# Kernel optimization log

Hardware: AMD Instinct MI355X
Metric: run time of the kernel (lower is better)

Reference implementation:

```python
import jax, jax.numpy as jnp
import numpy as np

NUM_HEADS = 4


def setup_inputs() -> dict:
    key = jax.random.key(0)
    ks = jax.random.split(key, 12)
    N, E_edges, ND, ED, D, G = 50000, 800000, 128, 64, 256, 128
    h = jax.random.normal(ks[0], (N, ND), dtype=jnp.float32)
    edge_index = jax.random.randint(ks[1], (2, E_edges), 0, N)
    edge_attr = jax.random.normal(ks[2], (E_edges, ED), dtype=jnp.float32)
    batch = jnp.sort(jax.random.randint(ks[3], (N,), 0, G))
    node_w = jax.random.normal(ks[4], (D, ND), dtype=jnp.float32) / np.sqrt(ND)
    node_b = jnp.zeros((D,), dtype=jnp.float32)
    edge_w = jax.random.normal(ks[5], (D, ED), dtype=jnp.float32) / np.sqrt(ED)
    edge_b = jnp.zeros((D,), dtype=jnp.float32)
    query = jax.random.normal(ks[6], (1, D), dtype=jnp.float32)
    in_w = jax.random.normal(ks[7], (3 * D, D), dtype=jnp.float32) / np.sqrt(D)
    in_b = jnp.zeros((3 * D,), dtype=jnp.float32)
    out_w = jax.random.normal(ks[8], (D, D), dtype=jnp.float32) / np.sqrt(D)
    out_b = jnp.zeros((D,), dtype=jnp.float32)
    return {"h": h, "edge_index": edge_index, "edge_attr": edge_attr, "batch": batch,
            "num_graphs": G, "node_w": node_w, "node_b": node_b,
            "edge_w": edge_w, "edge_b": edge_b, "query": query,
            "in_w": in_w, "in_b": in_b, "out_w": out_w, "out_b": out_b}


def reference(h, edge_index, edge_attr, batch, num_graphs,
              node_w, node_b, edge_w, edge_b, query, in_w, in_b, out_w, out_b):
    N = h.shape[0]
    D = query.shape[-1]
    dh = D // NUM_HEADS
    G = num_graphs
    # node projection
    h_proj = h @ node_w.T + node_b  # [N, D]
    # scatter-mean edge features to source nodes
    row = edge_index[0]
    e_proj = edge_attr @ edge_w.T + edge_b  # [E, D]
    e_sum = jax.ops.segment_sum(e_proj, row, num_segments=N)
    cnt = jax.ops.segment_sum(jnp.ones((row.shape[0],), jnp.float32), row, num_segments=N)
    h_proj = h_proj + e_sum / jnp.maximum(cnt, 1.0)[:, None]
    # per-graph single-query multi-head attention (torch MultiheadAttention math)
    wq, wk, wv = in_w[:D], in_w[D:2 * D], in_w[2 * D:]
    bq, bk, bv = in_b[:D], in_b[D:2 * D], in_b[2 * D:]
    q = (query @ wq.T + bq).reshape(NUM_HEADS, dh)            # [H, dh]
    k = (h_proj @ wk.T + bk).reshape(N, NUM_HEADS, dh)        # [N, H, dh]
    v = (h_proj @ wv.T + bv).reshape(N, NUM_HEADS, dh)        # [N, H, dh]
    scores = jnp.einsum('hd,nhd->nh', q, k) / jnp.sqrt(jnp.float32(dh))  # [N, H]
    smax = jax.ops.segment_max(scores, batch, num_segments=G)  # [G, H]
    w = jnp.exp(scores - smax[batch])                          # [N, H]
    denom = jax.ops.segment_sum(w, batch, num_segments=G)      # [G, H]
    p = w / jnp.maximum(denom[batch], 1e-30)                   # [N, H]
    pooled = jax.ops.segment_sum(p[:, :, None] * v, batch, num_segments=G)  # [G, H, dh]
    out = pooled.reshape(G, 1, D) @ out_w.T + out_b            # [G, 1, D]
    return out
```

## Files before the change

kernel.cpp:

```cpp
#include <hip/hip_runtime.h>
#include <hip/hip_bf16.h>
#include <math.h>

#define NDIM 128
#define EDIM 64
#define DDIM 256
#define BM 32
#define APK_STRIDE 204
#define HPB_STRIDE 264
#define NSPLIT 4
#define CAP 96
#define NSWZ (8 * 12 * 64 * 8)

typedef __attribute__((ext_vector_type(8))) short short8;
typedef __attribute__((ext_vector_type(16))) float floatx16;

__device__ inline ushort f2bf(float x) {
    uint32_t u = __float_as_uint(x);
    uint32_t r = (u + 0x7fff + ((u >> 16) & 1)) >> 16;
    return (ushort)r;
}
__device__ inline float bf2f(ushort h) { return __uint_as_float(((uint32_t)h) << 16); }
__device__ inline uint32_t pack_hilo(float x) {
    ushort hi = f2bf(x);
    ushort lo = f2bf(x - bf2f(hi));
    return (uint32_t)hi | ((uint32_t)lo << 16);
}

__global__ __launch_bounds__(256) void k_setup(
    int* __restrict__ zero_p, int n_zero, int ZBLK,
    const float* __restrict__ node_w, const float* __restrict__ edge_w,
    ushort* __restrict__ whi, ushort* __restrict__ wlo,
    const float* __restrict__ query, const float* __restrict__ in_w,
    const float* __restrict__ in_b, float* __restrict__ qk, float* __restrict__ sb)
{
    const int tid = threadIdx.x;
    int b = blockIdx.x;
    if (b < ZBLK) {
        int i = b * 256 + tid;
        if (i < n_zero) zero_p[i] = 0;
        return;
    }
    b -= ZBLK;
    if (b < 192) {
        int idx = b * 256 + tid;
        int i = idx & 7;
        int l = (idx >> 3) & 63;
        int rest = idx >> 9;
        int s = rest % 12;
        int t2 = rest / 12;
        int k = s * 16 + (l >> 5) * 8 + i;
        int col = t2 * 32 + (l & 31);
        float val = (k < NDIM) ? node_w[(size_t)col * NDIM + k]
                               : edge_w[(size_t)col * EDIM + (k - NDIM)];
        ushort hi = f2bf(val);
        ushort lo = f2bf(val - bf2f(hi));
        whi[idx] = hi;
        wlo[idx] = lo;
        return;
    }
    __shared__ float q_s[DDIM];
    __shared__ float qv[DDIM];
    q_s[tid] = query[tid];
    __syncthreads();
    float acc = in_b[tid];
    const float* wq = in_w + (size_t)tid * DDIM;
    for (int i = 0; i < DDIM; ++i) acc += q_s[i] * wq[i];
    qv[tid] = acc;
    __syncthreads();
    for (int h = 0; h < 4; ++h) {
        float a = 0.f;
        for (int d = 0; d < 64; ++d)
            a += qv[h * 64 + d] * in_w[(size_t)(DDIM + h * 64 + d) * DDIM + tid];
        qk[h * DDIM + tid] = a;
    }
    if (tid < 4) {
        float a = 0.f;
        for (int d = 0; d < 64; ++d) a += qv[tid * 64 + d] * in_b[DDIM + tid * 64 + d];
        sb[tid] = a;
    }
}

__global__ __launch_bounds__(256) void k_scatbin(
    const int* __restrict__ erow, const float* __restrict__ edge_attr,
    int* __restrict__ fill, ushort* __restrict__ ebin, int E)
{
    int gid = blockIdx.x * 256 + threadIdx.x;
    int e = gid >> 3;
    int seg8 = gid & 7;
    if (e >= E) return;
    int r = erow[e];
    int pos = 0;
    if (seg8 == 0) pos = atomicAdd(&fill[r], 1);
    pos = __shfl(pos, 0, 8);
    if (pos >= CAP) return;
    const float* ea = edge_attr + (size_t)e * EDIM + seg8 * 8;
    float4 va = *reinterpret_cast<const float4*>(ea);
    float4 vb = *reinterpret_cast<const float4*>(ea + 4);
    short8 o;
    o[0] = (short)f2bf(va.x); o[1] = (short)f2bf(va.y);
    o[2] = (short)f2bf(va.z); o[3] = (short)f2bf(va.w);
    o[4] = (short)f2bf(vb.x); o[5] = (short)f2bf(vb.y);
    o[6] = (short)f2bf(vb.z); o[7] = (short)f2bf(vb.w);
    *reinterpret_cast<short8*>(
        ebin + ((size_t)r * CAP + pos) * EDIM + seg8 * 8) = o;
}

__global__ __launch_bounds__(256) void k_projagg(
    const float* __restrict__ h, const ushort* __restrict__ ebin,
    const int* __restrict__ fill,
    const ushort* __restrict__ whi, const ushort* __restrict__ wlo,
    const float* __restrict__ node_b, const float* __restrict__ edge_b,
    const float* __restrict__ qk, const float* __restrict__ sb,
    ushort* __restrict__ h_proj_bf, float* __restrict__ scores, int N)
{
    extern __shared__ char smem[];
    uint32_t* A_pk = (uint32_t*)smem;
    ushort*   hpbuf = (ushort*)smem;
    __shared__ float qk_s[4 * DDIM];
    __shared__ float cnt_s[BM];
    __shared__ float sb_s[4];

    const int tid = threadIdx.x;
    const int n0 = blockIdx.x * BM;

    if (tid < BM) {
        int n = n0 + tid;
        cnt_s[tid] = (n < N) ? (float)fill[n] : 0.f;
    }
    if (tid < 4) sb_s[tid] = sb[tid];
    for (int i = tid; i < 4 * DDIM; i += 256) qk_s[i] = qk[i];

    const float4* h4 = reinterpret_cast<const float4*>(h);
#pragma unroll
    for (int it = 0; it < 4; ++it) {
        int idx4 = tid + 256 * it;
        int node = idx4 >> 5;
        int kq = idx4 & 31;
        float4 v = make_float4(0.f, 0.f, 0.f, 0.f);
        if (n0 + node < N) v = h4[(size_t)(n0 + node) * 32 + kq];
        uint32_t* dst = &A_pk[node * APK_STRIDE + kq * 4];
        dst[0] = pack_hilo(v.x); dst[1] = pack_hilo(v.y);
        dst[2] = pack_hilo(v.z); dst[3] = pack_hilo(v.w);
    }

    __syncthreads();

    {
        int node = tid >> 3;
        int seg8 = tid & 7;
        int n = n0 + node;
        float a[8];
#pragma unroll
        for (int i = 0; i < 8; ++i) a[i] = 0.f;
        if (n < N) {
            int c = min((int)cnt_s[node], CAP);
            const ushort* eb = ebin + ((size_t)n * CAP) * EDIM + seg8 * 8;
            int j = 0;
            for (; j + 3 < c; j += 4) {
                short8 v0 = *reinterpret_cast<const short8*>(eb + (size_t)(j + 0) * EDIM);
                short8 v1 = *reinterpret_cast<const short8*>(eb + (size_t)(j + 1) * EDIM);
                short8 v2 = *reinterpret_cast<const short8*>(eb + (size_t)(j + 2) * EDIM);
                short8 v3 = *reinterpret_cast<const short8*>(eb + (size_t)(j + 3) * EDIM);
#pragma unroll
                for (int i = 0; i < 8; ++i)
                    a[i] += (bf2f((ushort)v0[i]) + bf2f((ushort)v1[i]))
                          + (bf2f((ushort)v2[i]) + bf2f((ushort)v3[i]));
            }
            for (; j < c; ++j) {
                short8 v0 = *reinterpret_cast<const short8*>(eb + (size_t)j * EDIM);
#pragma unroll
                for (int i = 0; i < 8; ++i) a[i] += bf2f((ushort)v0[i]);
            }
        }
        float inv = 1.f / fmaxf(cnt_s[node], 1.f);
        uint32_t* dst = &A_pk[node * APK_STRIDE + NDIM + seg8 * 8];
#pragma unroll
        for (int i = 0; i < 8; ++i) dst[i] = pack_hilo(a[i] * inv);
    }
    __syncthreads();

    const int lane = tid & 63;
    const int w = tid >> 6;
    const int kg8 = (lane >> 5) * 8;
    const uint32_t* arow_p = &A_pk[(lane & 31) * APK_STRIDE];

    floatx16 acc[2];
#pragma unroll
    for (int t = 0; t < 2; ++t) acc[t] = 0.f;

#pragma unroll 4
    for (int s = 0; s < 12; ++s) {
        uint32_t au[8];
        *reinterpret_cast<uint4*>(&au[0]) = *reinterpret_cast<const uint4*>(&arow_p[s * 16 + kg8]);
        *reinterpret_cast<uint4*>(&au[4]) = *reinterpret_cast<const uint4*>(&arow_p[s * 16 + kg8 + 4]);
        short8 ahi, alo;
#pragma unroll
        for (int j = 0; j < 8; ++j) {
            ahi[j] = (short)(au[j] & 0xffffu);
            alo[j] = (short)(au[j] >> 16);
        }
#pragma unroll
        for (int t = 0; t < 2; ++t) {
            size_t boff = ((size_t)(((w * 2 + t) * 12 + s) * 64) + lane) * 8;
            short8 bhi = *reinterpret_cast<const short8*>(whi + boff);
            short8 blo = *reinterpret_cast<const short8*>(wlo + boff);
            acc[t] = __builtin_amdgcn_mfma_f32_32x32x16_bf16(ahi, bhi, acc[t], 0, 0, 0);
            acc[t] = __builtin_amdgcn_mfma_f32_32x32x16_bf16(ahi, blo, acc[t], 0, 0, 0);
            acc[t] = __builtin_amdgcn_mfma_f32_32x32x16_bf16(alo, bhi, acc[t], 0, 0, 0);
        }
    }
    __syncthreads();

#pragma unroll
    for (int t = 0; t < 2; ++t) {
        int colt = (w * 2 + t) * 32 + (lane & 31);
        float nb = node_b[colt];
        float eb = edge_b[colt];
#pragma unroll
        for (int r = 0; r < 16; ++r) {
            int row = (r & 3) + 8 * (r >> 2) + 4 * (lane >> 5);
            float fl = (cnt_s[row] >= 0.5f) ? 1.f : 0.f;
            float hp = acc[t][r] + nb + fl * eb;
            hpbuf[row * HPB_STRIDE + colt] = f2bf(hp);
        }
    }
    __syncthreads();

    {
        int row = tid >> 3, seg = tid & 7;
        int n = n0 + row;
        float s0 = 0.f, s1 = 0.f, s2 = 0.f, s3 = 0.f;
#pragma unroll
        for (int q = 0; q < 4; ++q) {
            short8 v = *reinterpret_cast<const short8*>(
                &hpbuf[row * HPB_STRIDE + seg * 32 + q * 8]);
#pragma unroll
            for (int jj = 0; jj < 8; ++jj) {
                float hv = bf2f((ushort)v[jj]);
                int dim = seg * 32 + q * 8 + jj;
                s0 += hv * qk_s[0 * DDIM + dim];
                s1 += hv * qk_s[1 * DDIM + dim];
                s2 += hv * qk_s[2 * DDIM + dim];
                s3 += hv * qk_s[3 * DDIM + dim];
            }
            if (n < N)
                *reinterpret_cast<short8*>(
                    &h_proj_bf[(size_t)n * DDIM + seg * 32 + q * 8]) = v;
        }
#pragma unroll
        for (int off = 1; off < 8; off <<= 1) {
            s0 += __shfl_xor(s0, off);
            s1 += __shfl_xor(s1, off);
            s2 += __shfl_xor(s2, off);
            s3 += __shfl_xor(s3, off);
        }
        if (seg == 0 && n < N) {
            scores[(size_t)n * 4 + 0] = (s0 + sb_s[0]) * 0.125f;
            scores[(size_t)n * 4 + 1] = (s1 + sb_s[1]) * 0.125f;
            scores[(size_t)n * 4 + 2] = (s2 + sb_s[2]) * 0.125f;
            scores[(size_t)n * 4 + 3] = (s3 + sb_s[3]) * 0.125f;
        }
    }
}

__global__ __launch_bounds__(256) void k_pool2(
    const ushort* __restrict__ h_proj_bf, const float* __restrict__ scores,
    const int* __restrict__ batch,
    float* __restrict__ pm, float* __restrict__ pd, float* __restrict__ phb, int N)
{
    __shared__ float sc_s[256 * 4];
    __shared__ float red_s[16];
    __shared__ float red[4][4][DDIM];

    const int b = blockIdx.x;
    const int g = b >> 2;
    const int part = b & 3;
    const int tid = threadIdx.x;
    const int lane = tid & 63;
    const int wave = tid >> 6;
    const int ng = tid >> 6;
    const int d0 = (tid & 63) * 4;

    int lo = 0, hi = N;
    while (lo < hi) { int mid = (lo + hi) >> 1; if (batch[mid] < g) lo = mid + 1; else hi = mid; }
    const int s = lo;
    hi = N;
    while (lo < hi) { int mid = (lo + hi) >> 1; if (batch[mid] < g + 1) lo = mid + 1; else hi = mid; }
    const int e = lo;
    const int len = e - s;
    const int cs = s + (len * part) / NSPLIT;
    const int ce = s + (len * (part + 1)) / NSPLIT;

    float m[4], dn[4];
    float hbv[4][4];
#pragma unroll
    for (int hh = 0; hh < 4; ++hh) {
        m[hh] = -INFINITY; dn[hh] = 0.f;
#pragma unroll
        for (int d = 0; d < 4; ++d) hbv[hh][d] = 0.f;
    }

    const int h = tid & 3;

    for (int c = cs; c < ce; c += 256) {
        int cn = min(256, ce - c);
        __syncthreads();
        if (tid < cn)
            *reinterpret_cast<float4*>(&sc_s[tid * 4]) =
                *reinterpret_cast<const float4*>(scores + (size_t)(c + tid) * 4);
        __syncthreads();

        float lm = -INFINITY;
        for (int n = tid >> 2; n < cn; n += 64) lm = fmaxf(lm, sc_s[n * 4 + h]);
#pragma unroll
        for (int off = 4; off < 64; off <<= 1) lm = fmaxf(lm, __shfl_xor(lm, off));
        if (lane < 4) red_s[wave * 4 + lane] = lm;
        __syncthreads();

        float nm[4];
#pragma unroll
        for (int hh = 0; hh < 4; ++hh) {
            float cm = fmaxf(fmaxf(red_s[hh], red_s[4 + hh]),
                             fmaxf(red_s[8 + hh], red_s[12 + hh]));
            nm[hh] = fmaxf(m[hh], cm);
            float sc = expf(m[hh] - nm[hh]);
            dn[hh] *= sc;
#pragma unroll
            for (int d = 0; d < 4; ++d) hbv[hh][d] *= sc;
            m[hh] = nm[hh];
        }
        __syncthreads();

        float mh = (h == 0) ? nm[0] : (h == 1) ? nm[1] : (h == 2) ? nm[2] : nm[3];
        float ld = 0.f;
        for (int idx = tid; idx < cn * 4; idx += 256) {
            float wv = expf(sc_s[idx] - mh);
            sc_s[idx] = wv;
            ld += wv;
        }
#pragma unroll
        for (int off = 4; off < 64; off <<= 1) ld += __shfl_xor(ld, off);
        __syncthreads();
        if (lane < 4) red_s[wave * 4 + lane] = ld;
        __syncthreads();
#pragma unroll
        for (int hh = 0; hh < 4; ++hh)
            dn[hh] += red_s[hh] + red_s[4 + hh] + red_s[8 + hh] + red_s[12 + hh];

#pragma unroll 2
        for (int nb = 0; nb < cn; nb += 4) {
            int ln = nb + ng;
            bool valid = ln < cn;
            float4 w4 = make_float4(0.f, 0.f, 0.f, 0.f);
            ushort4 hv = make_ushort4(0, 0, 0, 0);
            if (valid) {
                w4 = *reinterpret_cast<const float4*>(&sc_s[ln * 4]);
                hv = *reinterpret_cast<const ushort4*>(
                    &h_proj_bf[(size_t)(c + ln) * DDIM + d0]);
            }
            float vx = bf2f(hv.x), vy = bf2f(hv.y), vz = bf2f(hv.z), vw = bf2f(hv.w);
            hbv[0][0] += w4.x * vx; hbv[1][0] += w4.y * vx; hbv[2][0] += w4.z * vx; hbv[3][0] += w4.w * vx;
            hbv[0][1] += w4.x * vy; hbv[1][1] += w4.y * vy; hbv[2][1] += w4.z * vy; hbv[3][1] += w4.w * vy;
            hbv[0][2] += w4.x * vz; hbv[1][2] += w4.y * vz; hbv[2][2] += w4.z * vz; hbv[3][2] += w4.w * vz;
            hbv[0][3] += w4.x * vw; hbv[1][3] += w4.y * vw; hbv[2][3] += w4.z * vw; hbv[3][3] += w4.w * vw;
        }
    }

    __syncthreads();
#pragma unroll
    for (int hh = 0; hh < 4; ++hh)
#pragma unroll
        for (int d = 0; d < 4; ++d)
            red[ng][hh][d0 + d] = hbv[hh][d];
    __syncthreads();

    if (tid < 4) { pm[b * 4 + tid] = m[tid]; pd[b * 4 + tid] = dn[tid]; }
#pragma unroll
    for (int hh = 0; hh < 4; ++hh)
        phb[(size_t)(b * 4 + hh) * DDIM + tid] =
            red[0][hh][tid] + red[1][hh][tid] + red[2][hh][tid] + red[3][hh][tid];
}

__global__ __launch_bounds__(256) void k_out(
    const float* __restrict__ pm, const float* __restrict__ pd, const float* __restrict__ phb,
    const float* __restrict__ in_w, const float* __restrict__ in_b,
    const float* __restrict__ out_w, const float* __restrict__ out_b,
    float* __restrict__ out)
{
    __shared__ float hb_s[4 * DDIM];
    __shared__ float po_s[DDIM];

    const int g = blockIdx.x;
    const int tid = threadIdx.x;
    const int b0 = NSPLIT * g;

    float M[4], dnm[4], sc[NSPLIT][4];
#pragma unroll
    for (int hh = 0; hh < 4; ++hh) {
        float Mh = -INFINITY;
#pragma unroll
        for (int p = 0; p < NSPLIT; ++p) Mh = fmaxf(Mh, pm[(b0 + p) * 4 + hh]);
        M[hh] = Mh;
        float d = 0.f;
#pragma unroll
        for (int p = 0; p < NSPLIT; ++p) {
            float mp = pm[(b0 + p) * 4 + hh];
            float scp = (mp == -INFINITY) ? 0.f : expf(mp - Mh);
            sc[p][hh] = scp;
            d += pd[(b0 + p) * 4 + hh] * scp;
        }
        dnm[hh] = d;
    }
    const float has = (M[0] > -INFINITY) ? 1.f : 0.f;

#pragma unroll
    for (int hh = 0; hh < 4; ++hh) {
        float hb = 0.f;
#pragma unroll
        for (int p = 0; p < NSPLIT; ++p)
            hb += phb[(size_t)((b0 + p) * 4 + hh) * DDIM + tid] * sc[p][hh];
        hb_s[hh * DDIM + tid] = hb / fmaxf(dnm[hh], 1e-30f);
    }
    __syncthreads();

    const int jh = tid >> 6;
    const float* wv_row = in_w + (size_t)(2 * DDIM + tid) * DDIM;
    const float* hbr = &hb_s[jh * DDIM];
    float p = 0.f;
    for (int i = 0; i < DDIM; i += 4) {
        float4 a = *reinterpret_cast<const float4*>(hbr + i);
        float4 bb = *reinterpret_cast<const float4*>(wv_row + i);
        p += a.x * bb.x + a.y * bb.y + a.z * bb.z + a.w * bb.w;
    }
    p = (p + in_b[2 * DDIM + tid]) * has;
    po_s[tid] = p;
    __syncthreads();

    const float* ow_row = out_w + (size_t)tid * DDIM;
    float o = out_b[tid];
    for (int i = 0; i < DDIM; i += 4) {
        float4 a = *reinterpret_cast<const float4*>(&po_s[i]);
        float4 bb = *reinterpret_cast<const float4*>(ow_row + i);
        o += a.x * bb.x + a.y * bb.y + a.z * bb.z + a.w * bb.w;
    }
    out[(size_t)g * DDIM + tid] = o;
}

extern "C" void kernel_launch(void* const* d_in, const int* in_sizes, int n_in,
                              void* d_out, int out_size, void* d_ws, size_t ws_size,
                              hipStream_t stream) {
    const float* h         = (const float*)d_in[0];
    const int*   edge_idx  = (const int*)d_in[1];
    const float* edge_attr = (const float*)d_in[2];
    const int*   batch     = (const int*)d_in[3];
    const float* node_w    = (const float*)d_in[5];
    const float* node_b    = (const float*)d_in[6];
    const float* edge_w    = (const float*)d_in[7];
    const float* edge_b    = (const float*)d_in[8];
    const float* query     = (const float*)d_in[9];
    const float* in_w      = (const float*)d_in[10];
    const float* in_b      = (const float*)d_in[11];
    const float* out_w     = (const float*)d_in[12];
    const float* out_b     = (const float*)d_in[13];
    float* out = (float*)d_out;

    const int N = in_sizes[0] / NDIM;
    const int E = in_sizes[2] / EDIM;
    const int G = out_size / DDIM;

    char* ws = (char*)d_ws;
    size_t off = 0;
    auto alloc = [&](size_t bytes) { void* p = ws + off; off += (bytes + 255) & ~(size_t)255; return p; };

    int*    fill       = (int*)alloc((size_t)N * 4);
    ushort* h_proj_bf  = (ushort*)alloc((size_t)N * DDIM * 2);
    float*  scores     = (float*)alloc((size_t)N * 4 * 4);
    ushort* whi        = (ushort*)alloc((size_t)NSWZ * 2);
    ushort* wlo        = (ushort*)alloc((size_t)NSWZ * 2);
    float*  qk         = (float*)alloc(4 * DDIM * 4);
    float*  sb         = (float*)alloc(16 * 4);
    float*  pm         = (float*)alloc((size_t)NSPLIT * G * 4 * 4);
    float*  pd         = (float*)alloc((size_t)NSPLIT * G * 4 * 4);
    float*  phb        = (float*)alloc((size_t)NSPLIT * G * 4 * DDIM * 4);
    ushort* ebin       = (ushort*)alloc((size_t)N * CAP * EDIM * 2);

    const int ZBLK = (N + 255) / 256;
    k_setup<<<ZBLK + 192 + 1, 256, 0, stream>>>(
        fill, N, ZBLK, node_w, edge_w, whi, wlo, query, in_w, in_b, qk, sb);

    k_scatbin<<<((E * 8) + 255) / 256, 256, 0, stream>>>(
        edge_idx, edge_attr, fill, ebin, E);

    const int ldsA = BM * APK_STRIDE * 4;
    k_projagg<<<(N + BM - 1) / BM, 256, ldsA, stream>>>(
        h, ebin, fill, whi, wlo, node_b, edge_b, qk, sb,
        h_proj_bf, scores, N);

    k_pool2<<<NSPLIT * G, 256, 0, stream>>>(h_proj_bf, scores, batch, pm, pd, phb, N);
    k_out<<<G, 256, 0, stream>>>(pm, pd, phb, in_w, in_b, out_w, out_b, out);
}
```

Baseline: 211.9 us.

## Fold node/edge projections into scores and pooling to skip per-node GEMM

Uses linearity to drop the per-node MFMA projection to 256 dims. Scores are computed directly from raw h and the mean edge aggregate, dotted against query-key vectors pre-multiplied by node_w and edge_w. Pooling runs on raw h (128 dims) and the bf16 edge aggregate (64 dims), and the projection is applied once per graph in k_out. This removes the per-node GEMM and the 256-wide h_proj write and read. In exchange, k_out does more work per graph and pooling reads h again instead of a bf16 projected tensor.

```diff
diff --git a/kernel.cpp b/kernel.cpp
--- a/kernel.cpp
+++ b/kernel.cpp
@@ -5,15 +5,11 @@
 #define NDIM 128
 #define EDIM 64
 #define DDIM 256
-#define BM 32
-#define APK_STRIDE 204
-#define HPB_STRIDE 264
 #define NSPLIT 4
 #define CAP 96
-#define NSWZ (8 * 12 * 64 * 8)
+#define SNODES 32
 
 typedef __attribute__((ext_vector_type(8))) short short8;
-typedef __attribute__((ext_vector_type(16))) float floatx16;
 
 __device__ inline ushort f2bf(float x) {
     uint32_t u = __float_as_uint(x);
@@ -21,18 +17,13 @@
     return (ushort)r;
 }
 __device__ inline float bf2f(ushort h) { return __uint_as_float(((uint32_t)h) << 16); }
-__device__ inline uint32_t pack_hilo(float x) {
-    ushort hi = f2bf(x);
-    ushort lo = f2bf(x - bf2f(hi));
-    return (uint32_t)hi | ((uint32_t)lo << 16);
-}
 
 __global__ __launch_bounds__(256) void k_setup(
     int* __restrict__ zero_p, int n_zero, int ZBLK,
     const float* __restrict__ node_w, const float* __restrict__ edge_w,
-    ushort* __restrict__ whi, ushort* __restrict__ wlo,
+    const float* __restrict__ node_b, const float* __restrict__ edge_b,
     const float* __restrict__ query, const float* __restrict__ in_w,
-    const float* __restrict__ in_b, float* __restrict__ qk, float* __restrict__ sb)
+    const float* __restrict__ in_b, float* __restrict__ prep)
 {
     const int tid = threadIdx.x;
     int b = blockIdx.x;
@@ -41,26 +32,10 @@
         if (i < n_zero) zero_p[i] = 0;
         return;
     }
-    b -= ZBLK;
-    if (b < 192) {
-        int idx = b * 256 + tid;
-        int i = idx & 7;
-        int l = (idx >> 3) & 63;
-        int rest = idx >> 9;
-        int s = rest % 12;
-        int t2 = rest / 12;
-        int k = s * 16 + (l >> 5) * 8 + i;
-        int col = t2 * 32 + (l & 31);
-        float val = (k < NDIM) ? node_w[(size_t)col * NDIM + k]
-                               : edge_w[(size_t)col * EDIM + (k - NDIM)];
-        ushort hi = f2bf(val);
-        ushort lo = f2bf(val - bf2f(hi));
-        whi[idx] = hi;
-        wlo[idx] = lo;
-        return;
-    }
     __shared__ float q_s[DDIM];
     __shared__ float qv[DDIM];
+    __shared__ float qk_s[4 * DDIM];
+    __shared__ float sb_s[4];
     q_s[tid] = query[tid];
     __syncthreads();
     float acc = in_b[tid];
@@ -72,12 +47,34 @@
         float a = 0.f;
         for (int d = 0; d < 64; ++d)
             a += qv[h * 64 + d] * in_w[(size_t)(DDIM + h * 64 + d) * DDIM + tid];
-        qk[h * DDIM + tid] = a;
+        qk_s[h * DDIM + tid] = a;
     }
     if (tid < 4) {
         float a = 0.f;
         for (int d = 0; d < 64; ++d) a += qv[tid * 64 + d] * in_b[DDIM + tid * 64 + d];
-        sb[tid] = a;
+        sb_s[tid] = a;
+    }
+    __syncthreads();
+    for (int idx = tid; idx < 4 * NDIM; idx += 256) {
+        int hh = idx >> 7, k = idx & 127;
+        float a = 0.f;
+        for (int j = 0; j < DDIM; ++j) a += qk_s[hh * DDIM + j] * node_w[(size_t)j * NDIM + k];
+        prep[idx] = a;
+    }
+    {
+        int hh = tid >> 6, k = tid & 63;
+        float a = 0.f;
+        for (int j = 0; j < DDIM; ++j) a += qk_s[hh * DDIM + j] * edge_w[(size_t)j * EDIM + k];
+        prep[4 * NDIM + tid] = a;
+    }
+    if (tid < 4) {
+        float a = 0.f, e = 0.f;
+        for (int j = 0; j < DDIM; ++j) {
+            a += node_b[j] * qk_s[tid * DDIM + j];
+            e += edge_b[j] * qk_s[tid * DDIM + j];
+        }
+        prep[4 * NDIM + 256 + tid] = a + sb_s[tid];
+        prep[4 * NDIM + 260 + tid] = e;
     }
 }
 
@@ -106,172 +103,107 @@
         ebin + ((size_t)r * CAP + pos) * EDIM + seg8 * 8) = o;
 }
 
-__global__ __launch_bounds__(256) void k_projagg(
+__global__ __launch_bounds__(256) void k_score(
     const float* __restrict__ h, const ushort* __restrict__ ebin,
+    const int* __restrict__ fill, const float* __restrict__ prep,
+    ushort* __restrict__ agg_bf, float* __restrict__ scores, int N)
+{
+    __shared__ float qkn_s[4 * NDIM];
+    __shared__ float qke_s[4 * EDIM];
+    __shared__ float cst[8];
+    const int tid = threadIdx.x;
+    for (int i = tid; i < 4 * NDIM; i += 256) qkn_s[i] = prep[i];
+    qke_s[tid] = prep[4 * NDIM + tid];
+    if (tid < 8) cst[tid] = prep[4 * NDIM + 256 + tid];
+    __syncthreads();
+
+    const int node = blockIdx.x * SNODES + (tid >> 3);
+    const int seg8 = tid & 7;
+    if (node >= N) return;
+    const int cnt = fill[node];
+    const float inv = 1.f / fmaxf((float)cnt, 1.f);
+    const float fl = (cnt > 0) ? 1.f : 0.f;
+
+    float hd[4] = {0.f, 0.f, 0.f, 0.f};
+    const float4* hp = reinterpret_cast<const float4*>(h + (size_t)node * NDIM + seg8 * 16);
+#pragma unroll
+    for (int q = 0; q < 4; ++q) {
+        float4 hv = hp[q];
+        int base = seg8 * 16 + q * 4;
+#pragma unroll
+        for (int hh = 0; hh < 4; ++hh) {
+            const float* qp = &qkn_s[hh * NDIM + base];
+            hd[hh] += hv.x * qp[0] + hv.y * qp[1] + hv.z * qp[2] + hv.w * qp[3];
+        }
+    }
+
+    float a[8];
+#pragma unroll
+    for (int i = 0; i < 8; ++i) a[i] = 0.f;
+    {
+        const ushort* eb = ebin + (size_t)node * CAP * EDIM + seg8 * 8;
+        int c = min(cnt, CAP);
+        int j = 0;
+        for (; j + 3 < c; j += 4) {
+            short8 v0 = *reinterpret_cast<const short8*>(eb + (size_t)(j + 0) * EDIM);
+            short8 v1 = *reinterpret_cast<const short8*>(eb + (size_t)(j + 1) * EDIM);
+            short8 v2 = *reinterpret_cast<const short8*>(eb + (size_t)(j + 2) * EDIM);
+            short8 v3 = *reinterpret_cast<const short8*>(eb + (size_t)(j + 3) * EDIM);
+#pragma unroll
+            for (int i = 0; i < 8; ++i)
+                a[i] += (bf2f((ushort)v0[i]) + bf2f((ushort)v1[i]))
+                      + (bf2f((ushort)v2[i]) + bf2f((ushort)v3[i]));
+        }
+        for (; j < c; ++j) {
+            short8 v0 = *reinterpret_cast<const short8*>(eb + (size_t)j * EDIM);
+#pragma unroll
+            for (int i = 0; i < 8; ++i) a[i] += bf2f((ushort)v0[i]);
+        }
+    }
+    {
+        short8 o;
+#pragma unroll
+        for (int i = 0; i < 8; ++i) o[i] = (short)f2bf(a[i]);
+        *reinterpret_cast<short8*>(agg_bf + (size_t)node * EDIM + seg8 * 8) = o;
+    }
+    float ed[4] = {0.f, 0.f, 0.f, 0.f};
+#pragma unroll
+    for (int i = 0; i < 8; ++i) {
+#pragma unroll
+        for (int hh = 0; hh < 4; ++hh)
+            ed[hh] += a[i] * qke_s[hh * EDIM + seg8 * 8 + i];
+    }
+    float t[4];
+#pragma unroll
+    for (int hh = 0; hh < 4; ++hh) t[hh] = hd[hh] + ed[hh] * inv;
+#pragma unroll
+    for (int off = 1; off < 8; off <<= 1) {
+#pragma unroll
+        for (int hh = 0; hh < 4; ++hh) t[hh] += __shfl_xor(t[hh], off);
+    }
+    if (seg8 == 0) {
+        float4 sc;
+        sc.x = (t[0] + cst[0] + fl * cst[4]) * 0.125f;
+        sc.y = (t[1] + cst[1] + fl * cst[5]) * 0.125f;
+        sc.z = (t[2] + cst[2] + fl * cst[6]) * 0.125f;
+        sc.w = (t[3] + cst[3] + fl * cst[7]) * 0.125f;
+        *reinterpret_cast<float4*>(scores + (size_t)node * 4) = sc;
+    }
+}
+
+__global__ __launch_bounds__(256) void k_pool(
+    const float* __restrict__ h, const ushort* __restrict__ agg_bf,
+    const float* __restrict__ scores, const int* __restrict__ batch,
     const int* __restrict__ fill,
-    const ushort* __restrict__ whi, const ushort* __restrict__ wlo,
-    const float* __restrict__ node_b, const float* __restrict__ edge_b,
-    const float* __restrict__ qk, const float* __restrict__ sb,
-    ushort* __restrict__ h_proj_bf, float* __restrict__ scores, int N)
-{
-    extern __shared__ char smem[];
-    uint32_t* A_pk = (uint32_t*)smem;
-    ushort*   hpbuf = (ushort*)smem;
-    __shared__ float qk_s[4 * DDIM];
-    __shared__ float cnt_s[BM];
-    __shared__ float sb_s[4];
-
-    const int tid = threadIdx.x;
-    const int n0 = blockIdx.x * BM;
-
-    if (tid < BM) {
-        int n = n0 + tid;
-        cnt_s[tid] = (n < N) ? (float)fill[n] : 0.f;
-    }
-    if (tid < 4) sb_s[tid] = sb[tid];
-    for (int i = tid; i < 4 * DDIM; i += 256) qk_s[i] = qk[i];
-
-    const float4* h4 = reinterpret_cast<const float4*>(h);
-#pragma unroll
-    for (int it = 0; it < 4; ++it) {
-        int idx4 = tid + 256 * it;
-        int node = idx4 >> 5;
-        int kq = idx4 & 31;
-        float4 v = make_float4(0.f, 0.f, 0.f, 0.f);
-        if (n0 + node < N) v = h4[(size_t)(n0 + node) * 32 + kq];
-        uint32_t* dst = &A_pk[node * APK_STRIDE + kq * 4];
-        dst[0] = pack_hilo(v.x); dst[1] = pack_hilo(v.y);
-        dst[2] = pack_hilo(v.z); dst[3] = pack_hilo(v.w);
-    }
-
-    __syncthreads();
-
-    {
-        int node = tid >> 3;
-        int seg8 = tid & 7;
-        int n = n0 + node;
-        float a[8];
-#pragma unroll
-        for (int i = 0; i < 8; ++i) a[i] = 0.f;
-        if (n < N) {
-            int c = min((int)cnt_s[node], CAP);
-            const ushort* eb = ebin + ((size_t)n * CAP) * EDIM + seg8 * 8;
-            int j = 0;
-            for (; j + 3 < c; j += 4) {
-                short8 v0 = *reinterpret_cast<const short8*>(eb + (size_t)(j + 0) * EDIM);
-                short8 v1 = *reinterpret_cast<const short8*>(eb + (size_t)(j + 1) * EDIM);
-                short8 v2 = *reinterpret_cast<const short8*>(eb + (size_t)(j + 2) * EDIM);
-                short8 v3 = *reinterpret_cast<const short8*>(eb + (size_t)(j + 3) * EDIM);
-#pragma unroll
-                for (int i = 0; i < 8; ++i)
-                    a[i] += (bf2f((ushort)v0[i]) + bf2f((ushort)v1[i]))
-                          + (bf2f((ushort)v2[i]) + bf2f((ushort)v3[i]));
-            }
-            for (; j < c; ++j) {
-                short8 v0 = *reinterpret_cast<const short8*>(eb + (size_t)j * EDIM);
-#pragma unroll
-                for (int i = 0; i < 8; ++i) a[i] += bf2f((ushort)v0[i]);
-            }
-        }
-        float inv = 1.f / fmaxf(cnt_s[node], 1.f);
-        uint32_t* dst = &A_pk[node * APK_STRIDE + NDIM + seg8 * 8];
-#pragma unroll
-        for (int i = 0; i < 8; ++i) dst[i] = pack_hilo(a[i] * inv);
-    }
-    __syncthreads();
-
-    const int lane = tid & 63;
-    const int w = tid >> 6;
-    const int kg8 = (lane >> 5) * 8;
-    const uint32_t* arow_p = &A_pk[(lane & 31) * APK_STRIDE];
-
-    floatx16 acc[2];
-#pragma unroll
-    for (int t = 0; t < 2; ++t) acc[t] = 0.f;
-
-#pragma unroll 4
-    for (int s = 0; s < 12; ++s) {
-        uint32_t au[8];
-        *reinterpret_cast<uint4*>(&au[0]) = *reinterpret_cast<const uint4*>(&arow_p[s * 16 + kg8]);
-        *reinterpret_cast<uint4*>(&au[4]) = *reinterpret_cast<const uint4*>(&arow_p[s * 16 + kg8 + 4]);
-        short8 ahi, alo;
-#pragma unroll
-        for (int j = 0; j < 8; ++j) {
-            ahi[j] = (short)(au[j] & 0xffffu);
-            alo[j] = (short)(au[j] >> 16);
-        }
-#pragma unroll
-        for (int t = 0; t < 2; ++t) {
-            size_t boff = ((size_t)(((w * 2 + t) * 12 + s) * 64) + lane) * 8;
-            short8 bhi = *reinterpret_cast<const short8*>(whi + boff);
-            short8 blo = *reinterpret_cast<const short8*>(wlo + boff);
-            acc[t] = __builtin_amdgcn_mfma_f32_32x32x16_bf16(ahi, bhi, acc[t], 0, 0, 0);
-            acc[t] = __builtin_amdgcn_mfma_f32_32x32x16_bf16(ahi, blo, acc[t], 0, 0, 0);
-            acc[t] = __builtin_amdgcn_mfma_f32_32x32x16_bf16(alo, bhi, acc[t], 0, 0, 0);
-        }
-    }
-    __syncthreads();
-
-#pragma unroll
-    for (int t = 0; t < 2; ++t) {
-        int colt = (w * 2 + t) * 32 + (lane & 31);
-        float nb = node_b[colt];
-        float eb = edge_b[colt];
-#pragma unroll
-        for (int r = 0; r < 16; ++r) {
-            int row = (r & 3) + 8 * (r >> 2) + 4 * (lane >> 5);
-            float fl = (cnt_s[row] >= 0.5f) ? 1.f : 0.f;
-            float hp = acc[t][r] + nb + fl * eb;
-            hpbuf[row * HPB_STRIDE + colt] = f2bf(hp);
-        }
-    }
-    __syncthreads();
-
-    {
-        int row = tid >> 3, seg = tid & 7;
-        int n = n0 + row;
-        float s0 = 0.f, s1 = 0.f, s2 = 0.f, s3 = 0.f;
-#pragma unroll
-        for (int q = 0; q < 4; ++q) {
-            short8 v = *reinterpret_cast<const short8*>(
-                &hpbuf[row * HPB_STRIDE + seg * 32 + q * 8]);
-#pragma unroll
-            for (int jj = 0; jj < 8; ++jj) {
-                float hv = bf2f((ushort)v[jj]);
-                int dim = seg * 32 + q * 8 + jj;
-                s0 += hv * qk_s[0 * DDIM + dim];
-                s1 += hv * qk_s[1 * DDIM + dim];
-                s2 += hv * qk_s[2 * DDIM + dim];
-                s3 += hv * qk_s[3 * DDIM + dim];
-            }
-            if (n < N)
-                *reinterpret_cast<short8*>(
-                    &h_proj_bf[(size_t)n * DDIM + seg * 32 + q * 8]) = v;
-        }
-#pragma unroll
-        for (int off = 1; off < 8; off <<= 1) {
-            s0 += __shfl_xor(s0, off);
-            s1 += __shfl_xor(s1, off);
-            s2 += __shfl_xor(s2, off);
-            s3 += __shfl_xor(s3, off);
-        }
-        if (seg == 0 && n < N) {
-            scores[(size_t)n * 4 + 0] = (s0 + sb_s[0]) * 0.125f;
-            scores[(size_t)n * 4 + 1] = (s1 + sb_s[1]) * 0.125f;
-            scores[(size_t)n * 4 + 2] = (s2 + sb_s[2]) * 0.125f;
-            scores[(size_t)n * 4 + 3] = (s3 + sb_s[3]) * 0.125f;
-        }
-    }
-}
-
-__global__ __launch_bounds__(256) void k_pool2(
-    const ushort* __restrict__ h_proj_bf, const float* __restrict__ scores,
-    const int* __restrict__ batch,
-    float* __restrict__ pm, float* __restrict__ pd, float* __restrict__ phb, int N)
+    float* __restrict__ pm, float* __restrict__ pdn, float* __restrict__ pe,
+    float* __restrict__ pv, float* __restrict__ pu, int N)
 {
     __shared__ float sc_s[256 * 4];
-    __shared__ float red_s[16];
-    __shared__ float red[4][4][DDIM];
+    __shared__ float cn_s[256];
+    __shared__ float red_a[16];
+    __shared__ float red_b[16];
+    __shared__ float vred[2][4][NDIM];
+    __shared__ float ured[4][4][EDIM];
 
     const int b = blockIdx.x;
     const int g = b >> 2;
@@ -279,8 +211,10 @@
     const int tid = threadIdx.x;
     const int lane = tid & 63;
     const int wave = tid >> 6;
-    const int ng = tid >> 6;
-    const int d0 = (tid & 63) * 4;
+    const int dv = tid & 127;
+    const int g2 = tid >> 7;
+    const int du = tid & 63;
+    const int g4 = tid >> 6;
 
     int lo = 0, hi = N;
     while (lo < hi) { int mid = (lo + hi) >> 1; if (batch[mid] < g) lo = mid + 1; else hi = mid; }
@@ -292,102 +226,114 @@
     const int cs = s + (len * part) / NSPLIT;
     const int ce = s + (len * (part + 1)) / NSPLIT;
 
-    float m[4], dn[4];
-    float hbv[4][4];
+    float m[4], dn[4], spe[4], v[4], uh[4];
 #pragma unroll
     for (int hh = 0; hh < 4; ++hh) {
-        m[hh] = -INFINITY; dn[hh] = 0.f;
-#pragma unroll
-        for (int d = 0; d < 4; ++d) hbv[hh][d] = 0.f;
-    }
-
-    const int h = tid & 3;
+        m[hh] = -INFINITY; dn[hh] = 0.f; spe[hh] = 0.f; v[hh] = 0.f; uh[hh] = 0.f;
+    }
+
+    const int hsel = tid & 3;
 
     for (int c = cs; c < ce; c += 256) {
         int cn = min(256, ce - c);
         __syncthreads();
-        if (tid < cn)
+        if (tid < cn) {
             *reinterpret_cast<float4*>(&sc_s[tid * 4]) =
                 *reinterpret_cast<const float4*>(scores + (size_t)(c + tid) * 4);
+            cn_s[tid] = (float)fill[c + tid];
+        }
         __syncthreads();
 
         float lm = -INFINITY;
-        for (int n = tid >> 2; n < cn; n += 64) lm = fmaxf(lm, sc_s[n * 4 + h]);
+        for (int n = tid >> 2; n < cn; n += 64) lm = fmaxf(lm, sc_s[n * 4 + hsel]);
 #pragma unroll
         for (int off = 4; off < 64; off <<= 1) lm = fmaxf(lm, __shfl_xor(lm, off));
-        if (lane < 4) red_s[wave * 4 + lane] = lm;
+        if (lane < 4) red_a[wave * 4 + lane] = lm;
         __syncthreads();
 
         float nm[4];
 #pragma unroll
         for (int hh = 0; hh < 4; ++hh) {
-            float cm = fmaxf(fmaxf(red_s[hh], red_s[4 + hh]),
-                             fmaxf(red_s[8 + hh], red_s[12 + hh]));
+            float cm = fmaxf(fmaxf(red_a[hh], red_a[4 + hh]),
+                             fmaxf(red_a[8 + hh], red_a[12 + hh]));
             nm[hh] = fmaxf(m[hh], cm);
             float sc = expf(m[hh] - nm[hh]);
-            dn[hh] *= sc;
-#pragma unroll
-            for (int d = 0; d < 4; ++d) hbv[hh][d] *= sc;
+            dn[hh] *= sc; spe[hh] *= sc; v[hh] *= sc; uh[hh] *= sc;
             m[hh] = nm[hh];
         }
         __syncthreads();
 
-        float mh = (h == 0) ? nm[0] : (h == 1) ? nm[1] : (h == 2) ? nm[2] : nm[3];
-        float ld = 0.f;
+        float mh = (hsel == 0) ? nm[0] : (hsel == 1) ? nm[1] : (hsel == 2) ? nm[2] : nm[3];
+        float ld = 0.f, le = 0.f;
         for (int idx = tid; idx < cn * 4; idx += 256) {
             float wv = expf(sc_s[idx] - mh);
             sc_s[idx] = wv;
             ld += wv;
-        }
-#pragma unroll
-        for (int off = 4; off < 64; off <<= 1) ld += __shfl_xor(ld, off);
+            le += wv * ((cn_s[idx >> 2] > 0.5f) ? 1.f : 0.f);
+        }
+#pragma unroll
+        for (int off = 4; off < 64; off <<= 1) {
+            ld += __shfl_xor(ld, off);
+            le += __shfl_xor(le, off);
+        }
+        if (lane < 4) { red_a[wave * 4 + lane] = ld; red_b[wave * 4 + lane] = le; }
         __syncthreads();
-        if (lane < 4) red_s[wave * 4 + lane] = ld;
-        __syncthreads();
-#pragma unroll
-        for (int hh = 0; hh < 4; ++hh)
-            dn[hh] += red_s[hh] + red_s[4 + hh] + red_s[8 + hh] + red_s[12 + hh];
-
-#pragma unroll 2
-        for (int nb = 0; nb < cn; nb += 4) {
-            int ln = nb + ng;
-            bool valid = ln < cn;
-            float4 w4 = make_float4(0.f, 0.f, 0.f, 0.f);
-            ushort4 hv = make_ushort4(0, 0, 0, 0);
-            if (valid) {
-                w4 = *reinterpret_cast<const float4*>(&sc_s[ln * 4]);
-                hv = *reinterpret_cast<const ushort4*>(
-                    &h_proj_bf[(size_t)(c + ln) * DDIM + d0]);
-            }
-            float vx = bf2f(hv.x), vy = bf2f(hv.y), vz = bf2f(hv.z), vw = bf2f(hv.w);
-            hbv[0][0] += w4.x * vx; hbv[1][0] += w4.y * vx; hbv[2][0] += w4.z * vx; hbv[3][0] += w4.w * vx;
-            hbv[0][1] += w4.x * vy; hbv[1][1] += w4.y * vy; hbv[2][1] += w4.z * vy; hbv[3][1] += w4.w * vy;
-            hbv[0][2] += w4.x * vz; hbv[1][2] += w4.y * vz; hbv[2][2] += w4.z * vz; hbv[3][2] += w4.w * vz;
-            hbv[0][3] += w4.x * vw; hbv[1][3] += w4.y * vw; hbv[2][3] += w4.z * vw; hbv[3][3] += w4.w * vw;
-        }
-    }
-
-    __syncthreads();
-#pragma unroll
-    for (int hh = 0; hh < 4; ++hh)
-#pragma unroll
-        for (int d = 0; d < 4; ++d)
-            red[ng][hh][d0 + d] = hbv[hh][d];
-    __syncthreads();
-
-    if (tid < 4) { pm[b * 4 + tid] = m[tid]; pd[b * 4 + tid] = dn[tid]; }
-#pragma unroll
-    for (int hh = 0; hh < 4; ++hh)
-        phb[(size_t)(b * 4 + hh) * DDIM + tid] =
-            red[0][hh][tid] + red[1][hh][tid] + red[2][hh][tid] + red[3][hh][tid];
+#pragma unroll
+        for (int hh = 0; hh < 4; ++hh) {
+            dn[hh]  += red_a[hh] + red_a[4 + hh] + red_a[8 + hh] + red_a[12 + hh];
+            spe[hh] += red_b[hh] + red_b[4 + hh] + red_b[8 + hh] + red_b[12 + hh];
+        }
+
+        for (int ln = g2; ln < cn; ln += 2) {
+            float val = h[(size_t)(c + ln) * NDIM + dv];
+            float4 w4 = *reinterpret_cast<const float4*>(&sc_s[ln * 4]);
+            v[0] += w4.x * val; v[1] += w4.y * val;
+            v[2] += w4.z * val; v[3] += w4.w * val;
+        }
+        for (int ln = g4; ln < cn; ln += 4) {
+            float val = bf2f(agg_bf[(size_t)(c + ln) * EDIM + du]);
+            float ci = 1.f / fmaxf(cn_s[ln], 1.f);
+            float4 w4 = *reinterpret_cast<const float4*>(&sc_s[ln * 4]);
+            uh[0] += w4.x * ci * val; uh[1] += w4.y * ci * val;
+            uh[2] += w4.z * ci * val; uh[3] += w4.w * ci * val;
+        }
+    }
+
+    __syncthreads();
+#pragma unroll
+    for (int hh = 0; hh < 4; ++hh) {
+        vred[g2][hh][dv] = v[hh];
+        ured[g4][hh][du] = uh[hh];
+    }
+    __syncthreads();
+
+    if (tid < 4) { pm[b * 4 + tid] = m[tid]; pdn[b * 4 + tid] = dn[tid]; pe[b * 4 + tid] = spe[tid]; }
+    for (int idx = tid; idx < 4 * NDIM; idx += 256) {
+        int hh = idx >> 7, k = idx & 127;
+        pv[(size_t)(b * 4 + hh) * NDIM + k] = vred[0][hh][k] + vred[1][hh][k];
+    }
+    {
+        int hh = tid >> 6, k = tid & 63;
+        pu[(size_t)(b * 4 + hh) * EDIM + k] =
+            ured[0][hh][k] + ured[1][hh][k] + ured[2][hh][k] + ured[3][hh][k];
+    }
 }
 
 __global__ __launch_bounds__(256) void k_out(
-    const float* __restrict__ pm, const float* __restrict__ pd, const float* __restrict__ phb,
+    const float* __restrict__ pm, const float* __restrict__ pdn, const float* __restrict__ pe,
+    const float* __restrict__ pv, const float* __restrict__ pu,
+    const float* __restrict__ node_w, const float* __restrict__ edge_w,
+    const float* __restrict__ node_b, const float* __restrict__ edge_b,
     const float* __restrict__ in_w, const float* __restrict__ in_b,
     const float* __restrict__ out_w, const float* __restrict__ out_b,
     float* __restrict__ out)
 {
+    __shared__ float vm[4][NDIM];
+    __shared__ float um[4][EDIM];
+    __shared__ float scp_s[NSPLIT][4];
+    __shared__ float dnm_s[4];
+    __shared__ float spe_s[4];
+    __shared__ float has_s;
     __shared__ float hb_s[4 * DDIM];
     __shared__ float po_s[DDIM];
 
@@ -395,32 +341,70 @@
     const int tid = threadIdx.x;
     const int b0 = NSPLIT * g;
 
-    float M[4], dnm[4], sc[NSPLIT][4];
-#pragma unroll
-    for (int hh = 0; hh < 4; ++hh) {
+    if (tid < 4) {
         float Mh = -INFINITY;
 #pragma unroll
-        for (int p = 0; p < NSPLIT; ++p) Mh = fmaxf(Mh, pm[(b0 + p) * 4 + hh]);
-        M[hh] = Mh;
-        float d = 0.f;
+        for (int p = 0; p < NSPLIT; ++p) Mh = fmaxf(Mh, pm[(b0 + p) * 4 + tid]);
+        float d = 0.f, ee = 0.f;
 #pragma unroll
         for (int p = 0; p < NSPLIT; ++p) {
-            float mp = pm[(b0 + p) * 4 + hh];
+            float mp = pm[(b0 + p) * 4 + tid];
             float scp = (mp == -INFINITY) ? 0.f : expf(mp - Mh);
-            sc[p][hh] = scp;
-            d += pd[(b0 + p) * 4 + hh] * scp;
-        }
-        dnm[hh] = d;
-    }
-    const float has = (M[0] > -INFINITY) ? 1.f : 0.f;
-
-#pragma unroll
-    for (int hh = 0; hh < 4; ++hh) {
-        float hb = 0.f;
+            scp_s[p][tid] = scp;
+            d += pdn[(b0 + p) * 4 + tid] * scp;
+            ee += pe[(b0 + p) * 4 + tid] * scp;
+        }
+        dnm_s[tid] = d;
+        spe_s[tid] = ee;
+        if (tid == 0) has_s = (Mh > -INFINITY) ? 1.f : 0.f;
+    }
+    __syncthreads();
+
+    for (int idx = tid; idx < 4 * NDIM; idx += 256) {
+        int hh = idx >> 7, k = idx & 127;
+        float a = 0.f;
 #pragma unroll
         for (int p = 0; p < NSPLIT; ++p)
-            hb += phb[(size_t)((b0 + p) * 4 + hh) * DDIM + tid] * sc[p][hh];
-        hb_s[hh * DDIM + tid] = hb / fmaxf(dnm[hh], 1e-30f);
+            a += pv[(size_t)((b0 + p) * 4 + hh) * NDIM + k] * scp_s[p][hh];
+        vm[hh][k] = a;
+    }
+    {
+        int hh = tid >> 6, k = tid & 63;
+        float a = 0.f;
+#pragma unroll
+        for (int p = 0; p < NSPLIT; ++p)
+            a += pu[(size_t)((b0 + p) * 4 + hh) * EDIM + k] * scp_s[p][hh];
+        um[hh][k] = a;
+    }
+    __syncthreads();
+
+    {
+        int j = tid;
+        float acch[4];
+        float nbj = node_b[j], ebj = edge_b[j];
+#pragma unroll
+        for (int hh = 0; hh < 4; ++hh) acch[hh] = dnm_s[hh] * nbj + spe_s[hh] * ebj;
+        const float4* nwr = reinterpret_cast<const float4*>(node_w + (size_t)j * NDIM);
+        for (int q = 0; q < NDIM / 4; ++q) {
+            float4 w4 = nwr[q];
+#pragma unroll
+            for (int hh = 0; hh < 4; ++hh) {
+                const float* vp = &vm[hh][q * 4];
+                acch[hh] += w4.x * vp[0] + w4.y * vp[1] + w4.z * vp[2] + w4.w * vp[3];
+            }
+        }
+        const float4* ewr = reinterpret_cast<const float4*>(edge_w + (size_t)j * EDIM);
+        for (int q = 0; q < EDIM / 4; ++q) {
+            float4 w4 = ewr[q];
+#pragma unroll
+            for (int hh = 0; hh < 4; ++hh) {
+                const float* up = &um[hh][q * 4];
+                acch[hh] += w4.x * up[0] + w4.y * up[1] + w4.z * up[2] + w4.w * up[3];
+            }
+        }
+#pragma unroll
+        for (int hh = 0; hh < 4; ++hh)
+            hb_s[hh * DDIM + j] = acch[hh] / fmaxf(dnm_s[hh], 1e-30f);
     }
     __syncthreads();
 
@@ -433,7 +417,7 @@
         float4 bb = *reinterpret_cast<const float4*>(wv_row + i);
         p += a.x * bb.x + a.y * bb.y + a.z * bb.z + a.w * bb.w;
     }
-    p = (p + in_b[2 * DDIM + tid]) * has;
+    p = (p + in_b[2 * DDIM + tid]) * has_s;
     po_s[tid] = p;
     __syncthreads();
 
@@ -473,30 +457,31 @@
     size_t off = 0;
     auto alloc = [&](size_t bytes) { void* p = ws + off; off += (bytes + 255) & ~(size_t)255; return p; };
 
-    int*    fill       = (int*)alloc((size_t)N * 4);
-    ushort* h_proj_bf  = (ushort*)alloc((size_t)N * DDIM * 2);
-    float*  scores     = (float*)alloc((size_t)N * 4 * 4);
-    ushort* whi        = (ushort*)alloc((size_t)NSWZ * 2);
-    ushort* wlo        = (ushort*)alloc((size_t)NSWZ * 2);
-    float*  qk         = (float*)alloc(4 * DDIM * 4);
-    float*  sb         = (float*)alloc(16 * 4);
-    float*  pm         = (float*)alloc((size_t)NSPLIT * G * 4 * 4);
-    float*  pd         = (float*)alloc((size_t)NSPLIT * G * 4 * 4);
-    float*  phb        = (float*)alloc((size_t)NSPLIT * G * 4 * DDIM * 4);
-    ushort* ebin       = (ushort*)alloc((size_t)N * CAP * EDIM * 2);
+    int*    fill    = (int*)alloc((size_t)N * 4);
+    float*  scores  = (float*)alloc((size_t)N * 4 * 4);
+    ushort* agg_bf  = (ushort*)alloc((size_t)N * EDIM * 2);
+    float*  prep    = (float*)alloc(776 * 4);
+    float*  pm      = (float*)alloc((size_t)NSPLIT * G * 4 * 4);
+    float*  pdn     = (float*)alloc((size_t)NSPLIT * G * 4 * 4);
+    float*  pe      = (float*)alloc((size_t)NSPLIT * G * 4 * 4);
+    float*  pv      = (float*)alloc((size_t)NSPLIT * G * 4 * NDIM * 4);
+    float*  pu      = (float*)alloc((size_t)NSPLIT * G * 4 * EDIM * 4);
+    ushort* ebin    = (ushort*)alloc((size_t)N * CAP * EDIM * 2);
 
     const int ZBLK = (N + 255) / 256;
-    k_setup<<<ZBLK + 192 + 1, 256, 0, stream>>>(
-        fill, N, ZBLK, node_w, edge_w, whi, wlo, query, in_w, in_b, qk, sb);
+    k_setup<<<ZBLK + 1, 256, 0, stream>>>(
+        fill, N, ZBLK, node_w, edge_w, node_b, edge_b, query, in_w, in_b, prep);
 
     k_scatbin<<<((E * 8) + 255) / 256, 256, 0, stream>>>(
         edge_idx, edge_attr, fill, ebin, E);
 
-    const int ldsA = BM * APK_STRIDE * 4;
-    k_projagg<<<(N + BM - 1) / BM, 256, ldsA, stream>>>(
-        h, ebin, fill, whi, wlo, node_b, edge_b, qk, sb,
-        h_proj_bf, scores, N);
-
-    k_pool2<<<NSPLIT * G, 256, 0, stream>>>(h_proj_bf, scores, batch, pm, pd, phb, N);
-    k_out<<<G, 256, 0, stream>>>(pm, pd, phb, in_w, in_b, out_w, out_b, out);
-}
+    k_score<<<(N + SNODES - 1) / SNODES, 256, 0, stream>>>(
+        h, ebin, fill, prep, agg_bf, scores, N);
+
+    k_pool<<<NSPLIT * G, 256, 0, stream>>>(
+        h, agg_bf, scores, batch, fill, pm, pdn, pe, pv, pu, N);
+
+    k_out<<<G, 256, 0, stream>>>(
+        pm, pdn, pe, pv, pu, node_w, edge_w, node_b, edge_b,
+        in_w, in_b, out_w, out_b, out);
+}
```

Result: faster. 196.9 us (-7.1%).
